# Kernel optimization log

Hardware: AMD Instinct MI355X
Metric: run time of the kernel (lower is better)

## Reference

```python
import jax, jax.numpy as jnp
import numpy as np

B, S, D, H, FF = 4, 2048, 512, 8, 2048
W = 128  # local attention window size (hardcoded in module)
DH = D // H


def _ln(x, g, b, eps=1e-5):
    m = x.mean(-1, keepdims=True)
    v = ((x - m) ** 2).mean(-1, keepdims=True)
    return (x - m) / jnp.sqrt(v + eps) * g + b


def setup_inputs() -> dict:
    key = jax.random.key(0)
    ks = jax.random.split(key, 10)
    s = 0.02
    return {
        "src": jax.random.normal(ks[0], (B, S, D), jnp.float32),
        # global nn.MultiheadAttention params
        "in_proj_w": jax.random.normal(ks[1], (3 * D, D), jnp.float32) * s,
        "in_proj_b": jnp.zeros((3 * D,), jnp.float32),
        "out_proj_w": jax.random.normal(ks[2], (D, D), jnp.float32) * s,
        "out_proj_b": jnp.zeros((D,), jnp.float32),
        # LocalMHA params (prenorm LN, fused qkv no-bias, out proj no-bias)
        "ln_g": jnp.ones((D,), jnp.float32),
        "ln_b": jnp.zeros((D,), jnp.float32),
        "qkv_w": jax.random.normal(ks[3], (3 * D, D), jnp.float32) * s,
        "to_out_w": jax.random.normal(ks[4], (D, D), jnp.float32) * s,
        # glFusion + FFN + norms
        "gl_w": jax.random.normal(ks[5], (D, 2 * D), jnp.float32) * s,
        "gl_b": jnp.zeros((D,), jnp.float32),
        "norm1_g": jnp.ones((D,), jnp.float32),
        "norm1_b": jnp.zeros((D,), jnp.float32),
        "lin1_w": jax.random.normal(ks[6], (FF, D), jnp.float32) * s,
        "lin1_b": jnp.zeros((FF,), jnp.float32),
        "lin2_w": jax.random.normal(ks[7], (D, FF), jnp.float32) * s,
        "lin2_b": jnp.zeros((D,), jnp.float32),
        "norm2_g": jnp.ones((D,), jnp.float32),
        "norm2_b": jnp.zeros((D,), jnp.float32),
    }


def _forward(src, in_proj_w, in_proj_b, out_proj_w, out_proj_b, ln_g, ln_b,
             qkv_w, to_out_w, gl_w, gl_b, norm1_g, norm1_b,
             lin1_w, lin1_b, lin2_w, lin2_b, norm2_g, norm2_b):
    b, s, d = src.shape
    scale = DH ** -0.5

    def heads(x):  # (b, s, d) -> (b, H, s, DH)
        return x.reshape(b, s, H, DH).transpose(0, 2, 1, 3)

    # ---- global full MHA (no mask) ----
    qkv = src @ in_proj_w.T + in_proj_b
    qg, kg, vg = (heads(t) for t in jnp.split(qkv, 3, axis=-1))
    att = jax.nn.softmax(jnp.einsum('bhid,bhjd->bhij', qg, kg) * scale, axis=-1)
    go = jnp.einsum('bhij,bhjd->bhid', att, vg).transpose(0, 2, 1, 3).reshape(b, s, d)
    go = go @ out_proj_w.T + out_proj_b

    # ---- local windowed causal MHA with rotary (window=128, look_backward=1) ----
    x = _ln(src, ln_g, ln_b)  # prenorm
    ql, kl, vl = (heads(t) for t in jnp.split(x @ qkv_w.T, 3, axis=-1))

    pos = jnp.arange(s)
    inv_freq = 1.0 / (10000.0 ** (jnp.arange(0, DH, 2, dtype=jnp.float32) / DH))
    freqs = pos[:, None].astype(jnp.float32) * inv_freq[None, :]
    emb = jnp.concatenate([freqs, freqs], axis=-1)  # (s, DH)
    cos, sin = jnp.cos(emb), jnp.sin(emb)

    def rope(t):
        h = DH // 2
        t1, t2 = t[..., :h], t[..., h:]
        return t * cos + jnp.concatenate([-t2, t1], axis=-1) * sin

    ql, kl = rope(ql), rope(kl)
    ql = ql * scale

    nw = s // W
    qw = ql.reshape(b, H, nw, W, DH)
    kw = kl.reshape(b, H, nw, W, DH)
    vw = vl.reshape(b, H, nw, W, DH)

    def look_back(t):  # concat previous window with current: (b,H,nw,2W,DH)
        prev = jnp.pad(t, ((0, 0), (0, 0), (1, 0), (0, 0), (0, 0)))[:, :, :-1]
        return jnp.concatenate([prev, t], axis=3)

    bk, bv = look_back(kw), look_back(vw)

    qpos = pos.reshape(nw, W)
    kpos = jnp.concatenate(
        [jnp.concatenate([jnp.full((1, W), -1, pos.dtype), qpos[:-1]], axis=0), qpos],
        axis=1)  # (nw, 2W)
    mask = (kpos[:, None, :] >= 0) & (kpos[:, None, :] <= qpos[:, :, None])  # (nw,W,2W)

    sc = jnp.einsum('bhnid,bhnjd->bhnij', qw, bk)
    sc = jnp.where(mask, sc, jnp.finfo(sc.dtype).min)
    at = jax.nn.softmax(sc, axis=-1)
    lo = jnp.einsum('bhnij,bhnjd->bhnid', at, bv).reshape(b, H, s, DH)
    lo = lo.transpose(0, 2, 1, 3).reshape(b, s, d) @ to_out_w.T

    # ---- fuse global+local, residual, norms, FFN ----
    src2 = jnp.concatenate([go, lo], axis=-1) @ gl_w.T + gl_b
    h1 = _ln(src + src2, norm1_g, norm1_b)
    ff = jax.nn.relu(h1 @ lin1_w.T + lin1_b) @ lin2_w.T + lin2_b
    return _ln(h1 + ff, norm2_g, norm2_b)


def reference(src, in_proj_w, in_proj_b, out_proj_w, out_proj_b, ln_g, ln_b,
              qkv_w, to_out_w, gl_w, gl_b, norm1_g, norm1_b,
              lin1_w, lin1_b, lin2_w, lin2_b, norm2_g, norm2_b):
    return _forward(src, in_proj_w, in_proj_b, out_proj_w, out_proj_b, ln_g, ln_b,
                    qkv_w, to_out_w, gl_w, gl_b, norm1_g, norm1_b,
                    lin1_w, lin1_b, lin2_w, lin2_b, norm2_g, norm2_b)
```

## Files before the change

### kernel.cpp

```cpp
#include <hip/hip_runtime.h>
#include <math.h>

#define B_  4
#define S_  2048
#define D_  512
#define H_  8
#define FF_ 2048
#define W_  128
#define DH_ 64
#define NW_ 16
#define TRD (3*D_)
#define MR_ (B_*S_)

typedef __attribute__((ext_vector_type(8)))  short short8;
typedef __attribute__((ext_vector_type(4)))  short short4v;
typedef __attribute__((ext_vector_type(4)))  float f32x4;
typedef __attribute__((ext_vector_type(16))) float f32x16;

__device__ __forceinline__ short f2bf(float f) {
    unsigned u = __float_as_uint(f);
    unsigned r = (u + 0x7fff + ((u >> 16) & 1)) >> 16;
    return (short)r;
}
__device__ __forceinline__ float bf2f(ushort u) {
    return __uint_as_float(((unsigned)u) << 16);
}
__device__ __forceinline__ void gload_lds16(const ushort* g, short* l) {
    __builtin_amdgcn_global_load_lds(
        (const __attribute__((address_space(1))) void*)g,
        (__attribute__((address_space(3))) void*)l, 16, 0, 0);
}

struct CvtJobs { const float* s[8]; ushort* d[8]; int n[8]; };

__global__ __launch_bounds__(256) void cvt_kernel(CvtJobs jobs)
{
    int i4 = (blockIdx.x * 256 + threadIdx.x) * 4;
    #pragma unroll
    for (int j = 0; j < 8; j++) {
        if (i4 < jobs.n[j]) {
            float4 v = *(const float4*)(jobs.s[j] + i4);
            ushort4 o;
            o.x = (ushort)f2bf(v.x); o.y = (ushort)f2bf(v.y);
            o.z = (ushort)f2bf(v.z); o.w = (ushort)f2bf(v.w);
            *(ushort4*)(jobs.d[j] + i4) = o;
        }
    }
}

__global__ __launch_bounds__(256) void gemm_bf16_kernel(
    const ushort* __restrict__ A, int lda,
    const ushort* __restrict__ Wt,
    const float* __restrict__ bias,
    ushort* __restrict__ C, int ldc,
    int K, int relu)
{
    __shared__ short As[128 * 64];
    __shared__ short Bs[128 * 64];
    const int tid  = threadIdx.x;
    const int w    = tid >> 6;
    const int lane = tid & 63;
    const int quad = lane >> 4;
    const int x    = lane & 15;
    const int wr = w >> 1, wc = w & 1;
    const int bm = blockIdx.y * 128;
    const int bn = blockIdx.x * 128;

    const int srow = w * 32 + (lane >> 3);
    const int scol = ((lane & 7) ^ (lane >> 3)) * 8;

    f32x4 acc[4][4];
    #pragma unroll
    for (int i = 0; i < 4; i++)
        #pragma unroll
        for (int j = 0; j < 4; j++) acc[i][j] = (f32x4)0.f;

    for (int k0 = 0; k0 < K; k0 += 64) {
        __syncthreads();
        #pragma unroll
        for (int c = 0; c < 4; c++) {
            const ushort* ga = A + (size_t)(bm + srow + c * 8) * lda + k0 + scol;
            gload_lds16(ga, &As[(w * 32 + c * 8) * 64]);
            const ushort* gb = Wt + (size_t)(bn + srow + c * 8) * K + k0 + scol;
            gload_lds16(gb, &Bs[(w * 32 + c * 8) * 64]);
        }
        __syncthreads();

        #pragma unroll
        for (int kc = 0; kc < 2; kc++) {
            short8 af[4], bf[4];
            #pragma unroll
            for (int i = 0; i < 4; i++) {
                int row = wr * 64 + i * 16 + x;
                int pcg = (kc * 4 + quad) ^ (x & 7);
                af[i] = *(const short8*)&As[row * 64 + pcg * 8];
            }
            #pragma unroll
            for (int j = 0; j < 4; j++) {
                int row = wc * 64 + j * 16 + x;
                int pcg = (kc * 4 + quad) ^ (x & 7);
                bf[j] = *(const short8*)&Bs[row * 64 + pcg * 8];
            }
            #pragma unroll
            for (int i = 0; i < 4; i++)
                #pragma unroll
                for (int j = 0; j < 4; j++)
                    acc[i][j] = __builtin_amdgcn_mfma_f32_16x16x32_bf16(af[i], bf[j], acc[i][j], 0, 0, 0);
        }
    }

    #pragma unroll
    for (int i = 0; i < 4; i++) {
        #pragma unroll
        for (int r = 0; r < 4; r++) {
            size_t row = (size_t)(bm + wr * 64 + i * 16 + quad * 4 + r);
            #pragma unroll
            for (int j = 0; j < 4; j++) {
                int col = bn + wc * 64 + j * 16 + x;
                float v = acc[i][j][r] + (bias ? bias[col] : 0.f);
                if (relu) v = v > 0.f ? v : 0.f;
                C[row * ldc + col] = (ushort)f2bf(v);
            }
        }
    }
}

__device__ __forceinline__ float wave_sum64(float v) {
    #pragma unroll
    for (int off = 32; off > 0; off >>= 1) v += __shfl_xor(v, off, 64);
    return v;
}
__device__ __forceinline__ void load8(const float* p, float* v) {
    *(float4*)&v[0] = *(const float4*)p;
    *(float4*)&v[4] = *(const float4*)(p + 4);
}
__device__ __forceinline__ void load8(const ushort* p, float* v) {
    short8 s = *(const short8*)p;
    #pragma unroll
    for (int i = 0; i < 8; i++) v[i] = bf2f((ushort)s[i]);
}
__device__ __forceinline__ void store8(float* p, const float* v) {
    *(float4*)p       = make_float4(v[0], v[1], v[2], v[3]);
    *(float4*)(p + 4) = make_float4(v[4], v[5], v[6], v[7]);
}
__device__ __forceinline__ void store8(ushort* p, const float* v) {
    short8 s;
    #pragma unroll
    for (int i = 0; i < 8; i++) s[i] = f2bf(v[i]);
    *(short8*)p = s;
}

template <typename TA, typename TB, typename TO>
__global__ __launch_bounds__(256) void addln_kernel(
    const TA* __restrict__ a, const TB* __restrict__ b,
    const float* __restrict__ g, const float* __restrict__ be,
    TO* __restrict__ out)
{
    const int lane = threadIdx.x & 63;
    const int row  = blockIdx.x * 4 + (threadIdx.x >> 6);
    const size_t base = (size_t)row * D_ + lane * 8;
    float v[8];
    load8(a + base, v);
    if (b) {
        float wv[8];
        load8(b + base, wv);
        #pragma unroll
        for (int i = 0; i < 8; i++) v[i] += wv[i];
    }
    float s = 0.f;
    #pragma unroll
    for (int i = 0; i < 8; i++) s += v[i];
    float mean = wave_sum64(s) * (1.0f / 512.0f);
    float vs = 0.f;
    #pragma unroll
    for (int i = 0; i < 8; i++) { float d = v[i] - mean; vs += d * d; }
    float var = wave_sum64(vs) * (1.0f / 512.0f);
    float r = rsqrtf(var + 1e-5f);
    const int c = lane * 8;
    float t[8];
    #pragma unroll
    for (int i = 0; i < 8; i++) t[i] = (v[i] - mean) * r * g[c + i] + be[c + i];
    store8(out + base, t);
}

__global__ __launch_bounds__(256) void transpose_v_kernel(
    const ushort* __restrict__ qkv, ushort* __restrict__ vt)
{
    __shared__ ushort T[64][72];
    const int t  = threadIdx.x;
    const int s0 = blockIdx.x * 64;
    const int bh = blockIdx.y;
    const int b = bh >> 3, h = bh & 7;
    {
        int row = t >> 2, col = (t & 3) * 16;
        const ushort* src = qkv + ((size_t)(b * S_) + s0 + row) * TRD + 2 * D_ + h * DH_ + col;
        *(short8*)&T[row][col]     = *(const short8*)src;
        *(short8*)&T[row][col + 8] = *(const short8*)(src + 8);
    }
    __syncthreads();
    {
        int d = t >> 2, sc = (t & 3) * 16;
        ushort tmp[16];
        #pragma unroll
        for (int k = 0; k < 16; k++) tmp[k] = T[sc + k][d];
        ushort* dst = vt + ((size_t)bh * DH_ + d) * S_ + s0 + sc;
        *(short8*)dst       = *(const short8*)&tmp[0];
        *(short8*)(dst + 8) = *(const short8*)&tmp[8];
    }
}

#define PPW 72

template <int LOCAL>
__global__ __launch_bounds__(128) void attn_kernel(
    const ushort* __restrict__ qkv, const ushort* __restrict__ vt,
    ushort* __restrict__ out)
{
    __shared__ short Ks[64 * 64];
    __shared__ short Vt[64 * 64];
    __shared__ short Pb[2 * 32 * PPW];
    __shared__ float Lw[2][32];

    const int tid  = threadIdx.x;
    const int w    = tid >> 6;
    const int lane = tid & 63;
    const int half = lane >> 5;
    const int c    = lane & 31;
    const int bh = blockIdx.y;
    const int b = bh >> 3, h = bh & 7;
    const int qbase = blockIdx.x * 64;
    const size_t bS = (size_t)b * S_;
    const size_t vbase = (size_t)bh * DH_;

    short8 aq[4];
    {
        const ushort* qp = qkv + (bS + qbase + w * 32 + c) * TRD + h * DH_;
        #pragma unroll
        for (int kc = 0; kc < 4; kc++) {
            short8 raw = *(const short8*)(qp + kc * 16 + half * 8);
            if (LOCAL) {
                aq[kc] = raw;
            } else {
                #pragma unroll
                for (int j = 0; j < 8; j++)
                    aq[kc][j] = f2bf(bf2f((ushort)raw[j]) * 0.125f);
            }
        }
    }

    f32x16 ot[2];
    #pragma unroll
    for (int dt = 0; dt < 2; dt++) ot[dt] = (f32x16)0.f;
    float lp[16];
    #pragma unroll
    for (int r = 0; r < 16; r++) lp[r] = 0.f;

    short* Pw = &Pb[w * 32 * PPW];
    const int nkt = LOCAL ? 4 : (S_ / 64);

    for (int kt = 0; kt < nkt; kt++) {
        const int kbase = LOCAL ? ((qbase >> 7) * 128 - 128 + kt * 64) : kt * 64;
        if (LOCAL) {
            if (kbase < 0 || kbase > qbase + 63) continue;
        }
        const bool diag = LOCAL && (kbase == qbase);

        __syncthreads();
        #pragma unroll
        for (int cc = 0; cc < 4; cc++) {
            int row = w * 32 + cc * 8 + (lane >> 3);
            int cg  = (lane & 7) ^ (lane >> 3);
            const ushort* gk = qkv + (bS + kbase + row) * TRD + D_ + h * DH_ + cg * 8;
            gload_lds16(gk, &Ks[(w * 32 + cc * 8) * 64]);
            const ushort* gv = vt + (vbase + row) * S_ + kbase + cg * 8;
            gload_lds16(gv, &Vt[(w * 32 + cc * 8) * 64]);
        }
        __syncthreads();

        f32x16 sc[2];
        #pragma unroll
        for (int nt = 0; nt < 2; nt++) {
            sc[nt] = (f32x16)0.f;
            #pragma unroll
            for (int kc = 0; kc < 4; kc++) {
                int row = nt * 32 + c;
                int pcg = (kc * 2 + half) ^ (row & 7);
                short8 bk = *(const short8*)&Ks[row * 64 + pcg * 8];
                sc[nt] = __builtin_amdgcn_mfma_f32_32x32x16_bf16(aq[kc], bk, sc[nt], 0, 0, 0);
            }
        }

        #pragma unroll
        for (int nt = 0; nt < 2; nt++) {
            #pragma unroll
            for (int r = 0; r < 16; r++) {
                int qrow = (r & 3) + 8 * (r >> 2) + 4 * half;
                float p;
                if (diag) {
                    bool valid = (kbase + nt * 32 + c) <= (qbase + w * 32 + qrow);
                    p = valid ? __expf(sc[nt][r]) : 0.f;
                } else {
                    p = __expf(sc[nt][r]);
                }
                lp[r] += p;
                Pw[qrow * PPW + nt * 32 + c] = f2bf(p);
            }
        }
        asm volatile("s_waitcnt lgkmcnt(0)" ::: "memory");

        #pragma unroll
        for (int kc = 0; kc < 4; kc++) {
            short8 bp = *(const short8*)&Pw[c * PPW + kc * 16 + half * 8];
            #pragma unroll
            for (int dt = 0; dt < 2; dt++) {
                int row = dt * 32 + c;
                int pcg = (kc * 2 + half) ^ (row & 7);
                short8 av = *(const short8*)&Vt[row * 64 + pcg * 8];
                ot[dt] = __builtin_amdgcn_mfma_f32_32x32x16_bf16(av, bp, ot[dt], 0, 0, 0);
            }
        }
    }

    #pragma unroll
    for (int r = 0; r < 16; r++) {
        float v = lp[r];
        #pragma unroll
        for (int off = 1; off < 32; off <<= 1) v += __shfl_xor(v, off, 64);
        lp[r] = v;
    }
    if (c == 0) {
        #pragma unroll
        for (int r = 0; r < 16; r++)
            Lw[w][(r & 3) + 8 * (r >> 2) + 4 * half] = lp[r];
    }
    asm volatile("s_waitcnt lgkmcnt(0)" ::: "memory");
    __builtin_amdgcn_wave_barrier();
    float inv = 1.0f / Lw[w][c];

    #pragma unroll
    for (int dt = 0; dt < 2; dt++) {
        #pragma unroll
        for (int rq = 0; rq < 4; rq++) {
            short4v pk;
            #pragma unroll
            for (int i = 0; i < 4; i++)
                pk[i] = f2bf(ot[dt][rq * 4 + i] * inv);
            int dbase = dt * 32 + 8 * rq + 4 * half;
            *(short4v*)&Pw[c * PPW + dbase] = pk;
        }
    }
    asm volatile("s_waitcnt lgkmcnt(0)" ::: "memory");
    __builtin_amdgcn_wave_barrier();
    {
        int q  = lane >> 1;
        int d0 = (lane & 1) * 32;
        short8 v0 = *(const short8*)&Pw[q * PPW + d0];
        short8 v1 = *(const short8*)&Pw[q * PPW + d0 + 8];
        short8 v2 = *(const short8*)&Pw[q * PPW + d0 + 16];
        short8 v3 = *(const short8*)&Pw[q * PPW + d0 + 24];
        ushort* op = out + (bS + qbase + w * 32 + q) * D_ + h * DH_ + d0;
        *(short8*)(op)      = v0;
        *(short8*)(op + 8)  = v1;
        *(short8*)(op + 16) = v2;
        *(short8*)(op + 24) = v3;
    }
}

__global__ __launch_bounds__(256) void rope_kernel(ushort* __restrict__ qkv)
{
    int idx = blockIdx.x * 256 + threadIdx.x;
    int d  = idx & 31;
    int h  = (idx >> 5) & 7;
    int bs = idx >> 8;
    int pos = bs & (S_ - 1);
    float inv_freq = exp2f(-(float)d * (2.0f / 64.0f) * 13.287712379549449f);
    float ang = (float)pos * inv_freq;
    float sn, cs;
    sincosf(ang, &sn, &cs);
    ushort* base = qkv + (size_t)bs * TRD + h * DH_;
    float q1 = bf2f(base[d]), q2 = bf2f(base[d + 32]);
    base[d]      = (ushort)f2bf((q1 * cs - q2 * sn) * 0.125f);
    base[d + 32] = (ushort)f2bf((q2 * cs + q1 * sn) * 0.125f);
    ushort* kb = base + D_;
    float k1 = bf2f(kb[d]), k2 = bf2f(kb[d + 32]);
    kb[d]      = (ushort)f2bf(k1 * cs - k2 * sn);
    kb[d + 32] = (ushort)f2bf(k2 * cs + k1 * sn);
}

extern "C" void kernel_launch(void* const* d_in, const int* in_sizes, int n_in,
                              void* d_out, int out_size, void* d_ws, size_t ws_size,
                              hipStream_t stream)
{
    (void)in_sizes; (void)n_in; (void)out_size; (void)ws_size;
    const float* src        = (const float*)d_in[0];
    const float* in_proj_w  = (const float*)d_in[1];
    const float* in_proj_b  = (const float*)d_in[2];
    const float* out_proj_w = (const float*)d_in[3];
    const float* out_proj_b = (const float*)d_in[4];
    const float* ln_g       = (const float*)d_in[5];
    const float* ln_b       = (const float*)d_in[6];
    const float* qkv_w      = (const float*)d_in[7];
    const float* to_out_w   = (const float*)d_in[8];
    const float* gl_w       = (const float*)d_in[9];
    const float* gl_b       = (const float*)d_in[10];
    const float* norm1_g    = (const float*)d_in[11];
    const float* norm1_b    = (const float*)d_in[12];
    const float* lin1_w     = (const float*)d_in[13];
    const float* lin1_b     = (const float*)d_in[14];
    const float* lin2_w     = (const float*)d_in[15];
    const float* lin2_b     = (const float*)d_in[16];
    const float* norm2_g    = (const float*)d_in[17];
    const float* norm2_b    = (const float*)d_in[18];
    float* out = (float*)d_out;

    ushort* ws16   = (ushort*)d_ws;
    ushort* src_bf = ws16;
    ushort* wi_bf  = src_bf + (size_t)MR_ * D_;
    ushort* wq_bf  = wi_bf  + TRD * D_;
    ushort* wo_bf  = wq_bf  + TRD * D_;
    ushort* wt_bf  = wo_bf  + D_ * D_;
    ushort* wg_bf  = wt_bf  + D_ * D_;
    ushort* w1_bf  = wg_bf  + D_ * 2 * D_;
    ushort* w2_bf  = w1_bf  + FF_ * D_;
    ushort* buf1   = w2_bf  + D_ * FF_;
    ushort* h1b    = buf1   + (size_t)MR_ * D_;
    ushort* buf0   = h1b    + (size_t)MR_ * D_;
    ushort* buf2   = buf0   + (size_t)MR_ * TRD;
    ushort* vtg    = buf2   + (size_t)MR_ * 2 * D_;
    ushort* vtl    = vtg    + (size_t)MR_ * D_;
    ushort* ff1    = buf0;

    dim3 blk256(256), blk128(128);

    CvtJobs jobs;
    jobs.s[0] = src;        jobs.d[0] = src_bf; jobs.n[0] = MR_ * D_;
    jobs.s[1] = in_proj_w;  jobs.d[1] = wi_bf;  jobs.n[1] = TRD * D_;
    jobs.s[2] = qkv_w;      jobs.d[2] = wq_bf;  jobs.n[2] = TRD * D_;
    jobs.s[3] = out_proj_w; jobs.d[3] = wo_bf;  jobs.n[3] = D_ * D_;
    jobs.s[4] = to_out_w;   jobs.d[4] = wt_bf;  jobs.n[4] = D_ * D_;
    jobs.s[5] = gl_w;       jobs.d[5] = wg_bf;  jobs.n[5] = D_ * 2 * D_;
    jobs.s[6] = lin1_w;     jobs.d[6] = w1_bf;  jobs.n[6] = FF_ * D_;
    jobs.s[7] = lin2_w;     jobs.d[7] = w2_bf;  jobs.n[7] = D_ * FF_;
    cvt_kernel<<<dim3((MR_ * D_ / 4 + 255) / 256), blk256, 0, stream>>>(jobs);

    gemm_bf16_kernel<<<dim3(TRD / 128, MR_ / 128), blk256, 0, stream>>>(
        src_bf, D_, wi_bf, in_proj_b, buf0, TRD, D_, 0);
    transpose_v_kernel<<<dim3(S_ / 64, B_ * H_), blk256, 0, stream>>>(buf0, vtg);
    attn_kernel<0><<<dim3(S_ / 64, B_ * H_), blk128, 0, stream>>>(buf0, vtg, buf1);
    gemm_bf16_kernel<<<dim3(D_ / 128, MR_ / 128), blk256, 0, stream>>>(
        buf1, D_, wo_bf, out_proj_b, buf2, 2 * D_, D_, 0);
    addln_kernel<float, float, ushort><<<dim3(MR_ / 4), blk256, 0, stream>>>(
        src, (const float*)nullptr, ln_g, ln_b, buf1);
    gemm_bf16_kernel<<<dim3(TRD / 128, MR_ / 128), blk256, 0, stream>>>(
        buf1, D_, wq_bf, nullptr, buf0, TRD, D_, 0);
    transpose_v_kernel<<<dim3(S_ / 64, B_ * H_), blk256, 0, stream>>>(buf0, vtl);
    rope_kernel<<<dim3((B_ * S_ * H_ * 32) / 256), blk256, 0, stream>>>(buf0);
    attn_kernel<1><<<dim3(S_ / 64, B_ * H_), blk128, 0, stream>>>(buf0, vtl, buf1);
    gemm_bf16_kernel<<<dim3(D_ / 128, MR_ / 128), blk256, 0, stream>>>(
        buf1, D_, wt_bf, nullptr, buf2 + D_, 2 * D_, D_, 0);
    gemm_bf16_kernel<<<dim3(D_ / 128, MR_ / 128), blk256, 0, stream>>>(
        buf2, 2 * D_, wg_bf, gl_b, buf1, D_, 2 * D_, 0);
    addln_kernel<float, ushort, ushort><<<dim3(MR_ / 4), blk256, 0, stream>>>(
        src, buf1, norm1_g, norm1_b, h1b);
    gemm_bf16_kernel<<<dim3(FF_ / 128, MR_ / 128), blk256, 0, stream>>>(
        h1b, D_, w1_bf, lin1_b, ff1, FF_, D_, 1);
    gemm_bf16_kernel<<<dim3(D_ / 128, MR_ / 128), blk256, 0, stream>>>(
        ff1, FF_, w2_bf, lin2_b, buf1, D_, FF_, 0);
    addln_kernel<ushort, ushort, float><<<dim3(MR_ / 4), blk256, 0, stream>>>(
        h1b, buf1, norm2_g, norm2_b, out);
}
```

Baseline: 462.5 us.

## Fold output projections into fusion weights, split attention keys, shrink GEMM tiles

The global out_proj and local to_out weights are pre-multiplied into the glFusion weight, and the out_proj bias is folded into a fused bias. Attention now writes straight into the concat buffer, which removes two activation-sized GEMMs per call. The attention kernel moves to 256 threads that split the key range across wave pairs and reduce partial outputs through LDS. It keeps P in registers via lane shuffles instead of an LDS round trip, and uses truncating bf16 packing. GEMM tiles narrow to 128x64 for more blocks, at the cost of extra weight-precompute kernels per call and some rounding changes.

```diff
diff --git a/kernel.cpp b/kernel.cpp
--- a/kernel.cpp
+++ b/kernel.cpp
@@ -8,12 +8,11 @@
 #define FF_ 2048
 #define W_  128
 #define DH_ 64
-#define NW_ 16
 #define TRD (3*D_)
 #define MR_ (B_*S_)
+#define LDO_ 1024
 
 typedef __attribute__((ext_vector_type(8)))  short short8;
-typedef __attribute__((ext_vector_type(4)))  short short4v;
 typedef __attribute__((ext_vector_type(4)))  float f32x4;
 typedef __attribute__((ext_vector_type(16))) float f32x16;
 
@@ -24,6 +23,9 @@
 }
 __device__ __forceinline__ float bf2f(ushort u) {
     return __uint_as_float(((unsigned)u) << 16);
+}
+__device__ __forceinline__ unsigned pack_bf_trunc(float f0, float f1) {
+    return __builtin_amdgcn_perm(__float_as_uint(f1), __float_as_uint(f0), 0x07060302u);
 }
 __device__ __forceinline__ void gload_lds16(const ushort* g, short* l) {
     __builtin_amdgcn_global_load_lds(
@@ -56,7 +58,7 @@
     int K, int relu)
 {
     __shared__ short As[128 * 64];
-    __shared__ short Bs[128 * 64];
+    __shared__ short Bs[64 * 64];
     const int tid  = threadIdx.x;
     const int w    = tid >> 6;
     const int lane = tid & 63;
@@ -64,47 +66,45 @@
     const int x    = lane & 15;
     const int wr = w >> 1, wc = w & 1;
     const int bm = blockIdx.y * 128;
-    const int bn = blockIdx.x * 128;
-
-    const int srow = w * 32 + (lane >> 3);
+    const int bn = blockIdx.x * 64;
+
+    const int srow = (lane >> 3);
     const int scol = ((lane & 7) ^ (lane >> 3)) * 8;
 
-    f32x4 acc[4][4];
+    f32x4 acc[4][2];
     #pragma unroll
     for (int i = 0; i < 4; i++)
         #pragma unroll
-        for (int j = 0; j < 4; j++) acc[i][j] = (f32x4)0.f;
+        for (int j = 0; j < 2; j++) acc[i][j] = (f32x4)0.f;
 
     for (int k0 = 0; k0 < K; k0 += 64) {
         __syncthreads();
         #pragma unroll
         for (int c = 0; c < 4; c++) {
-            const ushort* ga = A + (size_t)(bm + srow + c * 8) * lda + k0 + scol;
+            const ushort* ga = A + (size_t)(bm + w * 32 + c * 8 + srow) * lda + k0 + scol;
             gload_lds16(ga, &As[(w * 32 + c * 8) * 64]);
-            const ushort* gb = Wt + (size_t)(bn + srow + c * 8) * K + k0 + scol;
-            gload_lds16(gb, &Bs[(w * 32 + c * 8) * 64]);
+        }
+        #pragma unroll
+        for (int c = 0; c < 2; c++) {
+            const ushort* gb = Wt + (size_t)(bn + w * 16 + c * 8 + srow) * K + k0 + scol;
+            gload_lds16(gb, &Bs[(w * 16 + c * 8) * 64]);
         }
         __syncthreads();
 
         #pragma unroll
         for (int kc = 0; kc < 2; kc++) {
-            short8 af[4], bf[4];
-            #pragma unroll
-            for (int i = 0; i < 4; i++) {
-                int row = wr * 64 + i * 16 + x;
-                int pcg = (kc * 4 + quad) ^ (x & 7);
-                af[i] = *(const short8*)&As[row * 64 + pcg * 8];
-            }
-            #pragma unroll
-            for (int j = 0; j < 4; j++) {
-                int row = wc * 64 + j * 16 + x;
-                int pcg = (kc * 4 + quad) ^ (x & 7);
-                bf[j] = *(const short8*)&Bs[row * 64 + pcg * 8];
-            }
+            short8 af[4], bf[2];
+            int pcg = (kc * 4 + quad) ^ (x & 7);
+            #pragma unroll
+            for (int i = 0; i < 4; i++)
+                af[i] = *(const short8*)&As[(wr * 64 + i * 16 + x) * 64 + pcg * 8];
+            #pragma unroll
+            for (int j = 0; j < 2; j++)
+                bf[j] = *(const short8*)&Bs[(wc * 32 + j * 16 + x) * 64 + pcg * 8];
             #pragma unroll
             for (int i = 0; i < 4; i++)
                 #pragma unroll
-                for (int j = 0; j < 4; j++)
+                for (int j = 0; j < 2; j++)
                     acc[i][j] = __builtin_amdgcn_mfma_f32_16x16x32_bf16(af[i], bf[j], acc[i][j], 0, 0, 0);
         }
     }
@@ -115,8 +115,8 @@
         for (int r = 0; r < 4; r++) {
             size_t row = (size_t)(bm + wr * 64 + i * 16 + quad * 4 + r);
             #pragma unroll
-            for (int j = 0; j < 4; j++) {
-                int col = bn + wc * 64 + j * 16 + x;
+            for (int j = 0; j < 2; j++) {
+                int col = bn + wc * 32 + j * 16 + x;
                 float v = acc[i][j][r] + (bias ? bias[col] : 0.f);
                 if (relu) v = v > 0.f ? v : 0.f;
                 C[row * ldc + col] = (ushort)f2bf(v);
@@ -209,160 +209,211 @@
     }
 }
 
-#define PPW 72
+__global__ __launch_bounds__(256) void transpose512_kernel(
+    const ushort* __restrict__ in, ushort* __restrict__ out)
+{
+    __shared__ ushort T[64][72];
+    const int t  = threadIdx.x;
+    const int r0 = blockIdx.y * 64, c0 = blockIdx.x * 64;
+    {
+        int row = t >> 2, col = (t & 3) * 16;
+        const ushort* s = in + (size_t)(r0 + row) * 512 + c0 + col;
+        *(short8*)&T[row][col]     = *(const short8*)s;
+        *(short8*)&T[row][col + 8] = *(const short8*)(s + 8);
+    }
+    __syncthreads();
+    {
+        int d = t >> 2, sc = (t & 3) * 16;
+        ushort tmp[16];
+        #pragma unroll
+        for (int k = 0; k < 16; k++) tmp[k] = T[sc + k][d];
+        ushort* dptr = out + (size_t)(c0 + d) * 512 + r0 + sc;
+        *(short8*)dptr       = *(const short8*)&tmp[0];
+        *(short8*)(dptr + 8) = *(const short8*)&tmp[8];
+    }
+}
+
+__global__ __launch_bounds__(256) void fuse_bias_kernel(
+    const float* __restrict__ gl_w, const float* __restrict__ opb,
+    const float* __restrict__ gl_b, float* __restrict__ bf)
+{
+    const int lane = threadIdx.x & 63;
+    const int row  = blockIdx.x * 4 + (threadIdx.x >> 6);
+    float s = 0.f;
+    #pragma unroll
+    for (int i = 0; i < 8; i++) {
+        int m = lane * 8 + i;
+        s += gl_w[(size_t)row * 1024 + m] * opb[m];
+    }
+    s = wave_sum64(s);
+    if (lane == 0) bf[row] = s + gl_b[row];
+}
 
 template <int LOCAL>
-__global__ __launch_bounds__(128) void attn_kernel(
+__global__ __launch_bounds__(256) void attn_kernel(
     const ushort* __restrict__ qkv, const ushort* __restrict__ vt,
-    ushort* __restrict__ out)
-{
-    __shared__ short Ks[64 * 64];
-    __shared__ short Vt[64 * 64];
-    __shared__ short Pb[2 * 32 * PPW];
-    __shared__ float Lw[2][32];
+    ushort* __restrict__ outp)
+{
+    __shared__ short KsS[2][64 * 64];
+    __shared__ short VtS[2][64 * 64];
+    __shared__ float Lw[4][32];
 
     const int tid  = threadIdx.x;
     const int w    = tid >> 6;
     const int lane = tid & 63;
-    const int half = lane >> 5;
+    const int hl   = lane >> 5;
     const int c    = lane & 31;
+    const int ks   = w >> 1;
+    const int qh   = w & 1;
     const int bh = blockIdx.y;
     const int b = bh >> 3, h = bh & 7;
     const int qbase = blockIdx.x * 64;
+    const int q0 = qbase + qh * 32;
     const size_t bS = (size_t)b * S_;
     const size_t vbase = (size_t)bh * DH_;
 
     short8 aq[4];
     {
-        const ushort* qp = qkv + (bS + qbase + w * 32 + c) * TRD + h * DH_;
+        const ushort* qp = qkv + (bS + q0 + c) * TRD + h * DH_;
         #pragma unroll
         for (int kc = 0; kc < 4; kc++) {
-            short8 raw = *(const short8*)(qp + kc * 16 + half * 8);
-            if (LOCAL) {
-                aq[kc] = raw;
-            } else {
+            short8 raw = *(const short8*)(qp + kc * 16 + hl * 8);
+            if (LOCAL) aq[kc] = raw;
+            else {
                 #pragma unroll
-                for (int j = 0; j < 8; j++)
-                    aq[kc][j] = f2bf(bf2f((ushort)raw[j]) * 0.125f);
+                for (int j = 0; j < 8; j++) aq[kc][j] = f2bf(bf2f((ushort)raw[j]) * 0.125f);
             }
         }
     }
 
     f32x16 ot[2];
-    #pragma unroll
-    for (int dt = 0; dt < 2; dt++) ot[dt] = (f32x16)0.f;
-    float lp[16];
-    #pragma unroll
-    for (int r = 0; r < 16; r++) lp[r] = 0.f;
-
-    short* Pw = &Pb[w * 32 * PPW];
-    const int nkt = LOCAL ? 4 : (S_ / 64);
-
-    for (int kt = 0; kt < nkt; kt++) {
-        const int kbase = LOCAL ? ((qbase >> 7) * 128 - 128 + kt * 64) : kt * 64;
-        if (LOCAL) {
-            if (kbase < 0 || kbase > qbase + 63) continue;
-        }
+    ot[0] = (f32x16)0.f; ot[1] = (f32x16)0.f;
+    float lp = 0.f;
+
+    const int NIT = LOCAL ? 2 : (S_ / 64 / 2);
+    for (int it = 0; it < NIT; it++) {
+        const int tile  = LOCAL ? (ks * 2 + it) : (ks * NIT + it);
+        const int kbase = LOCAL ? ((qbase >> 7) * 128 - 128 + tile * 64) : tile * 64;
+        const bool active = !LOCAL || (kbase >= 0 && kbase <= qbase + 63);
+        __syncthreads();
+        if (active) {
+            #pragma unroll
+            for (int cc = 0; cc < 4; cc++) {
+                int row = qh * 32 + cc * 8 + (lane >> 3);
+                int cg  = (lane & 7) ^ (lane >> 3);
+                gload_lds16(qkv + (bS + kbase + row) * TRD + D_ + h * DH_ + cg * 8,
+                            &KsS[ks][(qh * 32 + cc * 8) * 64]);
+                gload_lds16(vt + (vbase + row) * S_ + kbase + cg * 8,
+                            &VtS[ks][(qh * 32 + cc * 8) * 64]);
+            }
+        }
+        __syncthreads();
+        if (!active) continue;
         const bool diag = LOCAL && (kbase == qbase);
 
-        __syncthreads();
-        #pragma unroll
-        for (int cc = 0; cc < 4; cc++) {
-            int row = w * 32 + cc * 8 + (lane >> 3);
-            int cg  = (lane & 7) ^ (lane >> 3);
-            const ushort* gk = qkv + (bS + kbase + row) * TRD + D_ + h * DH_ + cg * 8;
-            gload_lds16(gk, &Ks[(w * 32 + cc * 8) * 64]);
-            const ushort* gv = vt + (vbase + row) * S_ + kbase + cg * 8;
-            gload_lds16(gv, &Vt[(w * 32 + cc * 8) * 64]);
-        }
-        __syncthreads();
-
-        f32x16 sc[2];
-        #pragma unroll
-        for (int nt = 0; nt < 2; nt++) {
-            sc[nt] = (f32x16)0.f;
-            #pragma unroll
-            for (int kc = 0; kc < 4; kc++) {
-                int row = nt * 32 + c;
-                int pcg = (kc * 2 + half) ^ (row & 7);
-                short8 bk = *(const short8*)&Ks[row * 64 + pcg * 8];
-                sc[nt] = __builtin_amdgcn_mfma_f32_32x32x16_bf16(aq[kc], bk, sc[nt], 0, 0, 0);
+        f32x16 e0 = (f32x16)0.f, e1 = (f32x16)0.f;
+        #pragma unroll
+        for (int kc = 0; kc < 4; kc++) {
+            int pcg = (kc * 2 + hl) ^ (c & 7);
+            short8 ak0 = *(const short8*)&KsS[ks][c * 64 + pcg * 8];
+            e0 = __builtin_amdgcn_mfma_f32_32x32x16_bf16(ak0, aq[kc], e0, 0, 0, 0);
+            short8 ak1 = *(const short8*)&KsS[ks][(32 + c) * 64 + pcg * 8];
+            e1 = __builtin_amdgcn_mfma_f32_32x32x16_bf16(ak1, aq[kc], e1, 0, 0, 0);
+        }
+
+        unsigned pk[2][8];
+        const int qi = q0 + c;
+        #pragma unroll
+        for (int mt = 0; mt < 2; mt++) {
+            f32x16& e = mt ? e1 : e0;
+            #pragma unroll
+            for (int r = 0; r < 16; r++) {
+                float p = __expf(e[r]);
+                if (diag) {
+                    int key = kbase + mt * 32 + (r & 3) + 8 * (r >> 2) + 4 * hl;
+                    if (key > qi) p = 0.f;
+                }
+                e[r] = p;
+                lp += p;
             }
-        }
-
-        #pragma unroll
-        for (int nt = 0; nt < 2; nt++) {
-            #pragma unroll
-            for (int r = 0; r < 16; r++) {
-                int qrow = (r & 3) + 8 * (r >> 2) + 4 * half;
-                float p;
-                if (diag) {
-                    bool valid = (kbase + nt * 32 + c) <= (qbase + w * 32 + qrow);
-                    p = valid ? __expf(sc[nt][r]) : 0.f;
-                } else {
-                    p = __expf(sc[nt][r]);
-                }
-                lp[r] += p;
-                Pw[qrow * PPW + nt * 32 + c] = f2bf(p);
-            }
-        }
-        asm volatile("s_waitcnt lgkmcnt(0)" ::: "memory");
+            #pragma unroll
+            for (int g = 0; g < 8; g++)
+                pk[mt][g] = pack_bf_trunc(e[2 * g], e[2 * g + 1]);
+        }
 
         #pragma unroll
         for (int kc = 0; kc < 4; kc++) {
-            short8 bp = *(const short8*)&Pw[c * PPW + kc * 16 + half * 8];
+            const int mt = kc >> 1, kp = kc & 1;
+            unsigned m0 = pk[mt][4 * kp + 0], m1 = pk[mt][4 * kp + 1];
+            unsigned m2 = pk[mt][4 * kp + 2], m3 = pk[mt][4 * kp + 3];
+            unsigned s0 = (unsigned)__shfl_xor((int)m0, 32, 64);
+            unsigned s1 = (unsigned)__shfl_xor((int)m1, 32, 64);
+            unsigned s2 = (unsigned)__shfl_xor((int)m2, 32, 64);
+            unsigned s3 = (unsigned)__shfl_xor((int)m3, 32, 64);
+            uint4 fd;
+            fd.x = hl ? s2 : m0;
+            fd.y = hl ? s3 : m1;
+            fd.z = hl ? m2 : s0;
+            fd.w = hl ? m3 : s1;
+            short8 bp = *(short8*)&fd;
             #pragma unroll
             for (int dt = 0; dt < 2; dt++) {
                 int row = dt * 32 + c;
-                int pcg = (kc * 2 + half) ^ (row & 7);
-                short8 av = *(const short8*)&Vt[row * 64 + pcg * 8];
+                int pcg = (kc * 2 + hl) ^ (c & 7);
+                short8 av = *(const short8*)&VtS[ks][row * 64 + pcg * 8];
                 ot[dt] = __builtin_amdgcn_mfma_f32_32x32x16_bf16(av, bp, ot[dt], 0, 0, 0);
             }
         }
     }
 
-    #pragma unroll
-    for (int r = 0; r < 16; r++) {
-        float v = lp[r];
-        #pragma unroll
-        for (int off = 1; off < 32; off <<= 1) v += __shfl_xor(v, off, 64);
-        lp[r] = v;
-    }
-    if (c == 0) {
-        #pragma unroll
-        for (int r = 0; r < 16; r++)
-            Lw[w][(r & 3) + 8 * (r >> 2) + 4 * half] = lp[r];
-    }
-    asm volatile("s_waitcnt lgkmcnt(0)" ::: "memory");
-    __builtin_amdgcn_wave_barrier();
-    float inv = 1.0f / Lw[w][c];
-
-    #pragma unroll
-    for (int dt = 0; dt < 2; dt++) {
-        #pragma unroll
-        for (int rq = 0; rq < 4; rq++) {
-            short4v pk;
-            #pragma unroll
-            for (int i = 0; i < 4; i++)
-                pk[i] = f2bf(ot[dt][rq * 4 + i] * inv);
-            int dbase = dt * 32 + 8 * rq + 4 * half;
-            *(short4v*)&Pw[c * PPW + dbase] = pk;
-        }
-    }
-    asm volatile("s_waitcnt lgkmcnt(0)" ::: "memory");
-    __builtin_amdgcn_wave_barrier();
-    {
-        int q  = lane >> 1;
-        int d0 = (lane & 1) * 32;
-        short8 v0 = *(const short8*)&Pw[q * PPW + d0];
-        short8 v1 = *(const short8*)&Pw[q * PPW + d0 + 8];
-        short8 v2 = *(const short8*)&Pw[q * PPW + d0 + 16];
-        short8 v3 = *(const short8*)&Pw[q * PPW + d0 + 24];
-        ushort* op = out + (bS + qbase + w * 32 + q) * D_ + h * DH_ + d0;
-        *(short8*)(op)      = v0;
-        *(short8*)(op + 8)  = v1;
-        *(short8*)(op + 16) = v2;
-        *(short8*)(op + 24) = v3;
+    lp += __shfl_xor(lp, 32, 64);
+    if (hl == 0) Lw[w][c] = lp;
+    __syncthreads();
+
+    float* scr = (float*)&KsS[0][0];
+    if (w >= 2) {
+        float* dst = scr + (w - 2) * 2048;
+        #pragma unroll
+        for (int dt = 0; dt < 2; dt++)
+            #pragma unroll
+            for (int r = 0; r < 16; r++)
+                dst[(dt * 16 + r) * 64 + lane] = ot[dt][r];
+    }
+    __syncthreads();
+    if (w < 2) {
+        const float* srcp = scr + w * 2048;
+        #pragma unroll
+        for (int dt = 0; dt < 2; dt++)
+            #pragma unroll
+            for (int r = 0; r < 16; r++)
+                ot[dt][r] += srcp[(dt * 16 + r) * 64 + lane];
+        float inv = 1.0f / (Lw[w][c] + Lw[w + 2][c]);
+
+        short* tr = (short*)&VtS[0][0] + w * 2304;
+        #pragma unroll
+        for (int dt = 0; dt < 2; dt++)
+            #pragma unroll
+            for (int rq = 0; rq < 4; rq++) {
+                uint2 pkv;
+                pkv.x = pack_bf_trunc(ot[dt][rq * 4 + 0] * inv, ot[dt][rq * 4 + 1] * inv);
+                pkv.y = pack_bf_trunc(ot[dt][rq * 4 + 2] * inv, ot[dt][rq * 4 + 3] * inv);
+                *(uint2*)&tr[c * 72 + dt * 32 + 8 * rq + 4 * hl] = pkv;
+            }
+        asm volatile("s_waitcnt lgkmcnt(0)" ::: "memory");
+        __builtin_amdgcn_wave_barrier();
+        {
+            int q  = lane >> 1;
+            int d0 = (lane & 1) * 32;
+            short8 v0 = *(const short8*)&tr[q * 72 + d0];
+            short8 v1 = *(const short8*)&tr[q * 72 + d0 + 8];
+            short8 v2 = *(const short8*)&tr[q * 72 + d0 + 16];
+            short8 v3 = *(const short8*)&tr[q * 72 + d0 + 24];
+            ushort* op = outp + (bS + q0 + q) * LDO_ + h * DH_ + d0;
+            *(short8*)(op)      = v0;
+            *(short8*)(op + 8)  = v1;
+            *(short8*)(op + 16) = v2;
+            *(short8*)(op + 24) = v3;
+        }
     }
 }
 
@@ -422,15 +473,18 @@
     ushort* wg_bf  = wt_bf  + D_ * D_;
     ushort* w1_bf  = wg_bf  + D_ * 2 * D_;
     ushort* w2_bf  = w1_bf  + FF_ * D_;
-    ushort* buf1   = w2_bf  + D_ * FF_;
+    ushort* opwT   = w2_bf  + D_ * FF_;
+    ushort* towT   = opwT   + D_ * D_;
+    ushort* wcat   = towT   + D_ * D_;
+    ushort* buf1   = wcat   + D_ * 2 * D_;
     ushort* h1b    = buf1   + (size_t)MR_ * D_;
     ushort* buf0   = h1b    + (size_t)MR_ * D_;
-    ushort* buf2   = buf0   + (size_t)MR_ * TRD;
-    ushort* vtg    = buf2   + (size_t)MR_ * 2 * D_;
-    ushort* vtl    = vtg    + (size_t)MR_ * D_;
+    ushort* cat    = buf0   + (size_t)MR_ * TRD;
+    ushort* vtb    = cat    + (size_t)MR_ * 2 * D_;
+    float*  bfuse  = (float*)(vtb + (size_t)MR_ * D_);
     ushort* ff1    = buf0;
 
-    dim3 blk256(256), blk128(128);
+    dim3 blk256(256);
 
     CvtJobs jobs;
     jobs.s[0] = src;        jobs.d[0] = src_bf; jobs.n[0] = MR_ * D_;
@@ -443,28 +497,32 @@
     jobs.s[7] = lin2_w;     jobs.d[7] = w2_bf;  jobs.n[7] = D_ * FF_;
     cvt_kernel<<<dim3((MR_ * D_ / 4 + 255) / 256), blk256, 0, stream>>>(jobs);
 
-    gemm_bf16_kernel<<<dim3(TRD / 128, MR_ / 128), blk256, 0, stream>>>(
+    transpose512_kernel<<<dim3(8, 8), blk256, 0, stream>>>(wo_bf, opwT);
+    transpose512_kernel<<<dim3(8, 8), blk256, 0, stream>>>(wt_bf, towT);
+    gemm_bf16_kernel<<<dim3(D_ / 64, D_ / 128), blk256, 0, stream>>>(
+        wg_bf, 2 * D_, opwT, nullptr, wcat, 2 * D_, D_, 0);
+    gemm_bf16_kernel<<<dim3(D_ / 64, D_ / 128), blk256, 0, stream>>>(
+        wg_bf + D_, 2 * D_, towT, nullptr, wcat + D_, 2 * D_, D_, 0);
+    fuse_bias_kernel<<<dim3(D_ / 4), blk256, 0, stream>>>(gl_w, out_proj_b, gl_b, bfuse);
+
+    gemm_bf16_kernel<<<dim3(TRD / 64, MR_ / 128), blk256, 0, stream>>>(
         src_bf, D_, wi_bf, in_proj_b, buf0, TRD, D_, 0);
-    transpose_v_kernel<<<dim3(S_ / 64, B_ * H_), blk256, 0, stream>>>(buf0, vtg);
-    attn_kernel<0><<<dim3(S_ / 64, B_ * H_), blk128, 0, stream>>>(buf0, vtg, buf1);
-    gemm_bf16_kernel<<<dim3(D_ / 128, MR_ / 128), blk256, 0, stream>>>(
-        buf1, D_, wo_bf, out_proj_b, buf2, 2 * D_, D_, 0);
+    transpose_v_kernel<<<dim3(S_ / 64, B_ * H_), blk256, 0, stream>>>(buf0, vtb);
+    attn_kernel<0><<<dim3(S_ / 64, B_ * H_), blk256, 0, stream>>>(buf0, vtb, cat);
     addln_kernel<float, float, ushort><<<dim3(MR_ / 4), blk256, 0, stream>>>(
         src, (const float*)nullptr, ln_g, ln_b, buf1);
-    gemm_bf16_kernel<<<dim3(TRD / 128, MR_ / 128), blk256, 0, stream>>>(
+    gemm_bf16_kernel<<<dim3(TRD / 64, MR_ / 128), blk256, 0, stream>>>(
         buf1, D_, wq_bf, nullptr, buf0, TRD, D_, 0);
-    transpose_v_kernel<<<dim3(S_ / 64, B_ * H_), blk256, 0, stream>>>(buf0, vtl);
+    transpose_v_kernel<<<dim3(S_ / 64, B_ * H_), blk256, 0, stream>>>(buf0, vtb);
     rope_kernel<<<dim3((B_ * S_ * H_ * 32) / 256), blk256, 0, stream>>>(buf0);
-    attn_kernel<1><<<dim3(S_ / 64, B_ * H_), blk128, 0, stream>>>(buf0, vtl, buf1);
-    gemm_bf16_kernel<<<dim3(D_ / 128, MR_ / 128), blk256, 0, stream>>>(
-        buf1, D_, wt_bf, nullptr, buf2 + D_, 2 * D_, D_, 0);
-    gemm_bf16_kernel<<<dim3(D_ / 128, MR_ / 128), blk256, 0, stream>>>(
-        buf2, 2 * D_, wg_bf, gl_b, buf1, D_, 2 * D_, 0);
+    attn_kernel<1><<<dim3(S_ / 64, B_ * H_), blk256, 0, stream>>>(buf0, vtb, cat + D_);
+    gemm_bf16_kernel<<<dim3(D_ / 64, MR_ / 128), blk256, 0, stream>>>(
+        cat, 2 * D_, wcat, bfuse, buf1, D_, 2 * D_, 0);
     addln_kernel<float, ushort, ushort><<<dim3(MR_ / 4), blk256, 0, stream>>>(
         src, buf1, norm1_g, norm1_b, h1b);
-    gemm_bf16_kernel<<<dim3(FF_ / 128, MR_ / 128), blk256, 0, stream>>>(
+    gemm_bf16_kernel<<<dim3(FF_ / 64, MR_ / 128), blk256, 0, stream>>>(
         h1b, D_, w1_bf, lin1_b, ff1, FF_, D_, 1);
-    gemm_bf16_kernel<<<dim3(D_ / 128, MR_ / 128), blk256, 0, stream>>>(
+    gemm_bf16_kernel<<<dim3(D_ / 64, MR_ / 128), blk256, 0, stream>>>(
         ff1, FF_, w2_bf, lin2_b, buf1, D_, FF_, 0);
     addln_kernel<ushort, ushort, float><<<dim3(MR_ / 4), blk256, 0, stream>>>(
         h1b, buf1, norm2_g, norm2_b, out);
```

After: 440.2 us. 4.8% less time.
